# Optimization experiments

Measured on AMD Instinct MI355X. Metric: run time of the kernel, lower is better.

The kernel has to match this reference:

```python
import jax, jax.numpy as jnp
import numpy as np
import math

N_NODES = 50000
N_EDGES = 1600000
HIDDEN = 128
HEADS = 4
HEAD_DIM = HIDDEN // HEADS


def setup_inputs() -> dict:
    key = jax.random.key(0)
    ks = jax.random.split(key, 10)
    s_in = 1.0 / math.sqrt(4)
    s_out = 1.0 / math.sqrt(HIDDEN)
    return {
        "x": jax.random.normal(ks[0], (N_NODES, 4), dtype=jnp.float32),
        "edge_index": jax.random.randint(ks[1], (2, N_EDGES), 0, N_NODES, dtype=jnp.int32),
        "Wq": jax.random.uniform(ks[2], (HIDDEN, 4), jnp.float32, -s_in, s_in),
        "bq": jax.random.uniform(ks[3], (HIDDEN,), jnp.float32, -s_in, s_in),
        "Wk": jax.random.uniform(ks[4], (HIDDEN, 4), jnp.float32, -s_in, s_in),
        "bk": jax.random.uniform(ks[5], (HIDDEN,), jnp.float32, -s_in, s_in),
        "Wv": jax.random.uniform(ks[6], (HIDDEN, 4), jnp.float32, -s_in, s_in),
        "bv": jax.random.uniform(ks[7], (HIDDEN,), jnp.float32, -s_in, s_in),
        "Wo": jax.random.uniform(ks[8], (4, HIDDEN), jnp.float32, -s_out, s_out),
        "bo": jax.random.uniform(ks[9], (4,), jnp.float32, -s_out, s_out),
    }


def reference(x, edge_index, Wq, bq, Wk, bk, Wv, bv, Wo, bo):
    n = x.shape[0]
    # projections 4 -> hidden, split into heads: [N, H, D]
    Q = (x @ Wq.T + bq).reshape(n, HEADS, HEAD_DIM)
    K = (x @ Wk.T + bk).reshape(n, HEADS, HEAD_DIM)
    V = (x @ Wv.T + bv).reshape(n, HEADS, HEAD_DIM)
    row, col = edge_index[0], edge_index[1]
    # per-edge, per-head scores: [E, H]
    scores = jnp.einsum('ehd,ehd->eh', Q[row], K[col]) / math.sqrt(HEAD_DIM)
    # NB: original applies softmax over ALL edges (dim=0), per head
    w = jax.nn.softmax(scores, axis=0)  # [E, H]
    # attended[col] += w * V[row]  -> segment-sum over destination nodes
    contrib = w[:, :, None] * V[row]  # [E, H, D]
    attended = jax.ops.segment_sum(contrib, col, num_segments=n)  # [N, H, D]
    attended = attended.reshape(n, HIDDEN)
    out = attended @ Wo.T + bo  # dropout is identity in eval
    return out + x
```

## Files before the change

kernel.cpp:

```cpp
#include <hip/hip_runtime.h>
#include <math.h>

#define NNODES 50000
#define NEDGES 1600000
#define BINSZ 128
#define NBINS 391
#define NBLK 1000
#define EPB (NEDGES / NBLK)
#define HALF 500
#define PCAP 2560
#define SCALE 0.17677669529663687f

__device__ __forceinline__ void compute_C_entry(int t,
        const float* Wq, const float* bq, const float* Wk, const float* bk,
        const float* Wv, const float* bv, const float* Wo, float* C_lds) {
    if (t < 64) {
        int h = t >> 4, a = (t >> 2) & 3, b = t & 3;
        float s = 0.f;
        for (int k = 0; k < 32; k++) s += Wq[(h * 32 + k) * 4 + a] * Wk[(h * 32 + k) * 4 + b];
        C_lds[t] = s;
    } else if (t < 80) {
        int h = (t - 64) >> 2, b = (t - 64) & 3;
        float s = 0.f;
        for (int k = 0; k < 32; k++) s += bq[h * 32 + k] * Wk[(h * 32 + k) * 4 + b];
        C_lds[t] = s;
    } else if (t < 96) {
        int h = (t - 80) >> 2, a = (t - 80) & 3;
        float s = 0.f;
        for (int k = 0; k < 32; k++) s += Wq[(h * 32 + k) * 4 + a] * bk[h * 32 + k];
        C_lds[t] = s;
    } else if (t < 100) {
        int h = t - 96;
        float s = 0.f;
        for (int k = 0; k < 32; k++) s += bq[h * 32 + k] * bk[h * 32 + k];
        C_lds[t] = s;
    } else if (t < 164) {
        int i = t - 100;
        int h = i >> 4, o = (i >> 2) & 3, a = i & 3;
        float s = 0.f;
        for (int k = 0; k < 32; k++) s += Wo[o * 128 + h * 32 + k] * Wv[(h * 32 + k) * 4 + a];
        C_lds[t] = s;
    } else if (t < 180) {
        int i = t - 164;
        int h = i >> 2, o = i & 3;
        float s = 0.f;
        for (int k = 0; k < 32; k++) s += Wo[o * 128 + h * 32 + k] * bv[h * 32 + k];
        C_lds[t] = s;
    }
}

__global__ __launch_bounds__(256) void k_binA(const int* __restrict__ ei,
                                              unsigned* __restrict__ chunks,
                                              unsigned* __restrict__ dir) {
    __shared__ unsigned raw[EPB];
    __shared__ unsigned srt[EPB];
    __shared__ int hist[512];
    __shared__ int ofs[512];
    int t = threadIdx.x, blk = blockIdx.x;
    hist[t] = 0; hist[t + 256] = 0;
    __syncthreads();
    int e0 = blk * EPB;
    for (int i = t; i < EPB; i += 256) {
        int r = ei[e0 + i];
        int c = ei[NEDGES + e0 + i];
        raw[i] = ((unsigned)c << 16) | (unsigned)r;
        atomicAdd(&hist[c >> 7], 1);
    }
    __syncthreads();
    if (t < 64) {
        int v[8], run = 0;
#pragma unroll
        for (int j = 0; j < 8; j++) { v[j] = hist[8 * t + j]; run += v[j]; }
        int p = run;
#pragma unroll
        for (int off = 1; off < 64; off <<= 1) {
            int u = __shfl_up(p, off, 64);
            if (t >= off) p += u;
        }
        int base = p - run;
#pragma unroll
        for (int j = 0; j < 8; j++) {
            hist[8 * t + j] = base;
            ofs[8 * t + j] = base;
            base += v[j];
        }
    }
    __syncthreads();
    for (int i = t; i < EPB; i += 256) {
        unsigned v = raw[i];
        int pos = atomicAdd(&ofs[v >> 23], 1);
        srt[pos] = v;
    }
    __syncthreads();
    uint4* co = (uint4*)(chunks + (size_t)blk * EPB);
    const uint4* si = (const uint4*)srt;
    for (int i = t; i < EPB / 4; i += 256) co[i] = si[i];
    for (int b = t; b < NBINS; b += 256) {
        int start = hist[b];
        int len = ofs[b] - start;
        dir[(size_t)blk * NBINS + b] = ((unsigned)start << 16) | (unsigned)len;
    }
}

__global__ __launch_bounds__(256) void k_tr(const unsigned* __restrict__ dir,
                                            unsigned* __restrict__ dirT) {
    __shared__ unsigned tile[32][33];
    int bi = blockIdx.x % 13;
    int bj = blockIdx.x / 13;
    int tx = threadIdx.x & 31, ty = threadIdx.x >> 5;
    int col = bi * 32 + tx;
#pragma unroll
    for (int k = 0; k < 4; k++) {
        int row = bj * 32 + ty + k * 8;
        if (row < NBLK && col < NBINS) tile[ty + k * 8][tx] = dir[(size_t)row * NBINS + col];
    }
    __syncthreads();
    int col2 = bj * 32 + tx;
#pragma unroll
    for (int k = 0; k < 4; k++) {
        int row2 = bi * 32 + ty + k * 8;
        if (row2 < NBINS && col2 < NBLK) dirT[(size_t)row2 * NBLK + col2] = tile[tx][ty + k * 8];
    }
}

__global__ __launch_bounds__(256) void k_accum(
        const unsigned* __restrict__ chunks, const unsigned* __restrict__ dirT,
        const float* __restrict__ x,
        const float* __restrict__ Wq, const float* __restrict__ bq,
        const float* __restrict__ Wk, const float* __restrict__ bk,
        const float* __restrict__ Wv, const float* __restrict__ bv,
        const float* __restrict__ Wo,
        float* __restrict__ acc, float* __restrict__ pS) {
    __shared__ float Cl[192];
    __shared__ float pe[BINSZ][20];
    __shared__ unsigned raw[PCAP];
    __shared__ unsigned short srt[PCAP];
    __shared__ int hist[BINSZ];
    __shared__ int ofs[BINSZ];
    __shared__ int runStart[HALF];
    __shared__ int srcBase[HALF];
    __shared__ int wsum[4];
    __shared__ float sw[4][4];
    int bid = blockIdx.x;
    int bin = bid >> 1;
    int part = bid & 1;
    int t = threadIdx.x;
    int base = bin << 7;
    compute_C_entry(t, Wq, bq, Wk, bk, Wv, bv, Wo, Cl);
    if (t < BINSZ) hist[t] = 0;
    __syncthreads();
    if (t < BINSZ) {
        int node = base + t;
        if (node < NNODES) {
            float4 xv = ((const float4*)x)[node];
            float pr[20];
#pragma unroll
            for (int h = 0; h < 4; h++) {
#pragma unroll
                for (int a = 0; a < 4; a++) {
                    float g = Cl[80 + h * 4 + a]
                            + Cl[h * 16 + a * 4 + 0] * xv.x + Cl[h * 16 + a * 4 + 1] * xv.y
                            + Cl[h * 16 + a * 4 + 2] * xv.z + Cl[h * 16 + a * 4 + 3] * xv.w;
                    pr[h * 4 + a] = g * SCALE;
                }
                float e = Cl[96 + h]
                        + Cl[64 + h * 4 + 0] * xv.x + Cl[64 + h * 4 + 1] * xv.y
                        + Cl[64 + h * 4 + 2] * xv.z + Cl[64 + h * 4 + 3] * xv.w;
                pr[16 + h] = e * SCALE;
            }
#pragma unroll
            for (int q = 0; q < 5; q++) ((float4*)pe[t])[q] = ((const float4*)pr)[q];
        }
    }
    uint2 dd = {0u, 0u};
    int cnt = 0;
    if (t < HALF / 2) {
        dd = *(const uint2*)(dirT + (size_t)bin * NBLK + part * HALF + 2 * t);
        cnt = (int)(dd.x & 0xFFFFu) + (int)(dd.y & 0xFFFFu);
    }
    int lane = t & 63, w = t >> 6;
    int p = cnt;
#pragma unroll
    for (int off = 1; off < 64; off <<= 1) {
        int u = __shfl_up(p, off, 64);
        if (lane >= off) p += u;
    }
    if (lane == 63) wsum[w] = p;
    __syncthreads();
    int wbase = 0;
#pragma unroll
    for (int ww = 0; ww < 4; ww++) wbase += (ww < w) ? wsum[ww] : 0;
    int off0 = wbase + p - cnt;
    int nval = wsum[0] + wsum[1] + wsum[2] + wsum[3];
    if (nval > PCAP) nval = PCAP;
    if (t < HALF / 2) {
        int len0 = (int)(dd.x & 0xFFFFu);
        runStart[2 * t] = off0;
        runStart[2 * t + 1] = off0 + len0;
        srcBase[2 * t] = (part * HALF + 2 * t) * EPB + (int)(dd.x >> 16);
        srcBase[2 * t + 1] = (part * HALF + 2 * t + 1) * EPB + (int)(dd.y >> 16);
    }
    __syncthreads();
    for (int i = t; i < nval; i += 256) {
        int lo = 0, hi = HALF;
        while (hi - lo > 1) {
            int mid = (lo + hi) >> 1;
            if (runStart[mid] <= i) lo = mid; else hi = mid;
        }
        unsigned v = chunks[srcBase[lo] + (i - runStart[lo])];
        raw[i] = v;
        atomicAdd(&hist[(int)(v >> 16) - base], 1);
    }
    __syncthreads();
    if (t < 64) {
        int a0 = hist[2 * t], a1 = hist[2 * t + 1];
        int pair = a0 + a1;
        int pp = pair;
#pragma unroll
        for (int off = 1; off < 64; off <<= 1) {
            int u = __shfl_up(pp, off, 64);
            if (t >= off) pp += u;
        }
        int excl = pp - pair;
        hist[2 * t] = excl; hist[2 * t + 1] = excl + a0;
        ofs[2 * t] = excl;  ofs[2 * t + 1] = excl + a0;
    }
    __syncthreads();
    for (int i = t; i < nval; i += 256) {
        unsigned v = raw[i];
        int lc = (int)(v >> 16) - base;
        int pos = atomicAdd(&ofs[lc], 1);
        srt[pos] = (unsigned short)(v & 0xFFFFu);
    }
    __syncthreads();
    int nl = t >> 1;
    int sub = t & 1;
    int node = base + nl;
    int sBeg = hist[nl], sEnd = ofs[nl];
    float4 g0 = ((const float4*)pe[nl])[0];
    float4 g1 = ((const float4*)pe[nl])[1];
    float4 g2 = ((const float4*)pe[nl])[2];
    float4 g3 = ((const float4*)pe[nl])[3];
    float4 eh = ((const float4*)pe[nl])[4];
    float S0 = 0.f, S1 = 0.f, S2 = 0.f, S3 = 0.f;
    float4 y0 = {0, 0, 0, 0}, y1 = y0, y2 = y0, y3 = y0;
    for (int i = sBeg + sub; i < sEnd; i += 2) {
        int r = (int)srt[i];
        float4 xv = ((const float4*)x)[r];
        float p0 = __expf(xv.x * g0.x + xv.y * g0.y + xv.z * g0.z + xv.w * g0.w + eh.x);
        float p1 = __expf(xv.x * g1.x + xv.y * g1.y + xv.z * g1.z + xv.w * g1.w + eh.y);
        float p2 = __expf(xv.x * g2.x + xv.y * g2.y + xv.z * g2.z + xv.w * g2.w + eh.z);
        float p3 = __expf(xv.x * g3.x + xv.y * g3.y + xv.z * g3.z + xv.w * g3.w + eh.w);
        y0.x += p0 * xv.x; y0.y += p0 * xv.y; y0.z += p0 * xv.z; y0.w += p0 * xv.w;
        y1.x += p1 * xv.x; y1.y += p1 * xv.y; y1.z += p1 * xv.z; y1.w += p1 * xv.w;
        y2.x += p2 * xv.x; y2.y += p2 * xv.y; y2.z += p2 * xv.z; y2.w += p2 * xv.w;
        y3.x += p3 * xv.x; y3.y += p3 * xv.y; y3.z += p3 * xv.z; y3.w += p3 * xv.w;
        S0 += p0; S1 += p1; S2 += p2; S3 += p3;
    }
    y0.x += __shfl_xor(y0.x, 1); y0.y += __shfl_xor(y0.y, 1);
    y0.z += __shfl_xor(y0.z, 1); y0.w += __shfl_xor(y0.w, 1);
    y1.x += __shfl_xor(y1.x, 1); y1.y += __shfl_xor(y1.y, 1);
    y1.z += __shfl_xor(y1.z, 1); y1.w += __shfl_xor(y1.w, 1);
    y2.x += __shfl_xor(y2.x, 1); y2.y += __shfl_xor(y2.y, 1);
    y2.z += __shfl_xor(y2.z, 1); y2.w += __shfl_xor(y2.w, 1);
    y3.x += __shfl_xor(y3.x, 1); y3.y += __shfl_xor(y3.y, 1);
    y3.z += __shfl_xor(y3.z, 1); y3.w += __shfl_xor(y3.w, 1);
    S0 += __shfl_xor(S0, 1); S1 += __shfl_xor(S1, 1);
    S2 += __shfl_xor(S2, 1); S3 += __shfl_xor(S3, 1);
    if (node < NNODES) {
        float4* ap = (float4*)(acc + ((size_t)part * NNODES + node) * 20);
        float4 sv = {S0, S1, S2, S3};
        if (sub == 0) { ap[0] = y0; ap[2] = y2; ap[4] = sv; }
        else { ap[1] = y1; ap[3] = y3; }
    }
    float z0 = (sub == 0 && node < NNODES) ? S0 : 0.f;
    float z1 = (sub == 0 && node < NNODES) ? S1 : 0.f;
    float z2 = (sub == 0 && node < NNODES) ? S2 : 0.f;
    float z3 = (sub == 0 && node < NNODES) ? S3 : 0.f;
#pragma unroll
    for (int off = 1; off < 64; off <<= 1) {
        z0 += __shfl_xor(z0, off); z1 += __shfl_xor(z1, off);
        z2 += __shfl_xor(z2, off); z3 += __shfl_xor(z3, off);
    }
    if ((t & 63) == 0) { sw[w][0] = z0; sw[w][1] = z1; sw[w][2] = z2; sw[w][3] = z3; }
    __syncthreads();
    if (t == 0) {
        float4 v;
        v.x = sw[0][0] + sw[1][0] + sw[2][0] + sw[3][0];
        v.y = sw[0][1] + sw[1][1] + sw[2][1] + sw[3][1];
        v.z = sw[0][2] + sw[1][2] + sw[2][2] + sw[3][2];
        v.w = sw[0][3] + sw[1][3] + sw[2][3] + sw[3][3];
        ((float4*)pS)[bid] = v;
    }
}

__global__ __launch_bounds__(256) void k_out(
        const float* __restrict__ acc, const float* __restrict__ pS,
        const float* __restrict__ Wq, const float* __restrict__ bq,
        const float* __restrict__ Wk, const float* __restrict__ bk,
        const float* __restrict__ Wv, const float* __restrict__ bv,
        const float* __restrict__ Wo, const float* __restrict__ bo,
        const float* __restrict__ x, float* __restrict__ out) {
    __shared__ float Cl[192];
    __shared__ float sd[4][4];
    __shared__ float dd[4];
    int t = threadIdx.x;
    compute_C_entry(t, Wq, bq, Wk, bk, Wv, bv, Wo, Cl);
    float s0 = 0.f, s1 = 0.f, s2 = 0.f, s3 = 0.f;
    for (int i = t; i < 2 * NBINS; i += 256) {
        float4 v = ((const float4*)pS)[i];
        s0 += v.x; s1 += v.y; s2 += v.z; s3 += v.w;
    }
#pragma unroll
    for (int off = 1; off < 64; off <<= 1) {
        s0 += __shfl_xor(s0, off); s1 += __shfl_xor(s1, off);
        s2 += __shfl_xor(s2, off); s3 += __shfl_xor(s3, off);
    }
    int w = t >> 6;
    if ((t & 63) == 0) { sd[w][0] = s0; sd[w][1] = s1; sd[w][2] = s2; sd[w][3] = s3; }
    __syncthreads();
    if (t < 4) dd[t] = 1.f / (sd[0][t] + sd[1][t] + sd[2][t] + sd[3][t]);
    __syncthreads();
    int i = blockIdx.x * blockDim.x + t;
    if (i >= NNODES) return;
    const float4* a0 = (const float4*)(acc + (size_t)i * 20);
    const float4* a1 = (const float4*)(acc + ((size_t)NNODES + i) * 20);
    float4 y[4], S;
#pragma unroll
    for (int q = 0; q < 4; q++) {
        float4 u = a0[q], v = a1[q];
        y[q].x = u.x + v.x; y[q].y = u.y + v.y; y[q].z = u.z + v.z; y[q].w = u.w + v.w;
    }
    {
        float4 u = a0[4], v = a1[4];
        S.x = u.x + v.x; S.y = u.y + v.y; S.z = u.z + v.z; S.w = u.w + v.w;
    }
    float Sv[4] = {S.x, S.y, S.z, S.w};
    float di[4] = {dd[0], dd[1], dd[2], dd[3]};
    float o[4];
#pragma unroll
    for (int oo = 0; oo < 4; oo++) {
        float a = bo[oo];
#pragma unroll
        for (int h = 0; h < 4; h++) {
            float m = Cl[100 + h * 16 + oo * 4 + 0] * y[h].x
                    + Cl[100 + h * 16 + oo * 4 + 1] * y[h].y
                    + Cl[100 + h * 16 + oo * 4 + 2] * y[h].z
                    + Cl[100 + h * 16 + oo * 4 + 3] * y[h].w
                    + Cl[164 + h * 4 + oo] * Sv[h];
            a += di[h] * m;
        }
        o[oo] = a;
    }
    float4 xv = ((const float4*)x)[i];
    float4 ov;
    ov.x = o[0] + xv.x; ov.y = o[1] + xv.y; ov.z = o[2] + xv.z; ov.w = o[3] + xv.w;
    ((float4*)out)[i] = ov;
}

extern "C" void kernel_launch(void* const* d_in, const int* in_sizes, int n_in,
                              void* d_out, int out_size, void* d_ws, size_t ws_size,
                              hipStream_t stream) {
    const float* x = (const float*)d_in[0];
    const int* ei = (const int*)d_in[1];
    const float* Wq = (const float*)d_in[2];
    const float* bq = (const float*)d_in[3];
    const float* Wk = (const float*)d_in[4];
    const float* bk = (const float*)d_in[5];
    const float* Wv = (const float*)d_in[6];
    const float* bv = (const float*)d_in[7];
    const float* Wo = (const float*)d_in[8];
    const float* bo = (const float*)d_in[9];
    float* out = (float*)d_out;

    float* fws = (float*)d_ws;
    float* acc = fws;
    float* pS = acc + (size_t)2 * NNODES * 20;
    unsigned* chunks = (unsigned*)(pS + (size_t)2 * NBINS * 4 + 4);
    unsigned* dir = chunks + (size_t)NEDGES;
    unsigned* dirT = dir + (size_t)NBLK * NBINS;

    k_binA<<<NBLK, 256, 0, stream>>>(ei, chunks, dir);
    k_tr<<<13 * 32, 256, 0, stream>>>(dir, dirT);
    k_accum<<<2 * NBINS, 256, 0, stream>>>(chunks, dirT, x, Wq, bq, Wk, bk, Wv, bv, Wo, acc, pS);
    k_out<<<(NNODES + 255) / 256, 256, 0, stream>>>(acc, pS,
                                                    Wq, bq, Wk, bk, Wv, bv, Wo, bo, x, out);
}
```

Baseline: 52.78 us.

## Split accumulation into CSR-build kernel and node-split accumulate kernel

Before, each bin was split across two blocks by source-block half, and both partial results went to separate accumulator copies. Now a new kernel gathers every edge of a bin into a per-bin CSR, and the accumulate kernel splits a bin by node halves with four threads per node. The Q/K projections move into the transpose kernel, writing a global proj buffer. This drops the duplicate accumulator reads in k_out and the per-element binary search, at the cost of an extra launch and a CSR round-trip through global memory.

```diff
diff --git a/kernel.cpp b/kernel.cpp
--- a/kernel.cpp
+++ b/kernel.cpp
@@ -7,8 +7,8 @@
 #define NBINS 391
 #define NBLK 1000
 #define EPB (NEDGES / NBLK)
-#define HALF 500
-#define PCAP 2560
+#define CAPB 4864
+#define STRIP 19
 #define SCALE 0.17677669529663687f
 
 __device__ __forceinline__ void compute_C_entry(int t,
@@ -102,12 +102,18 @@
     }
 }
 
-__global__ __launch_bounds__(256) void k_tr(const unsigned* __restrict__ dir,
-                                            unsigned* __restrict__ dirT) {
+__global__ __launch_bounds__(256) void k_prep(const unsigned* __restrict__ dir,
+        unsigned* __restrict__ dirT, const float* __restrict__ x,
+        const float* __restrict__ Wq, const float* __restrict__ bq,
+        const float* __restrict__ Wk, const float* __restrict__ bk,
+        const float* __restrict__ Wv, const float* __restrict__ bv,
+        const float* __restrict__ Wo, float* __restrict__ proj) {
     __shared__ unsigned tile[32][33];
+    __shared__ float Cl[192];
+    int t = threadIdx.x;
     int bi = blockIdx.x % 13;
     int bj = blockIdx.x / 13;
-    int tx = threadIdx.x & 31, ty = threadIdx.x >> 5;
+    int tx = t & 31, ty = t >> 5;
     int col = bi * 32 + tx;
 #pragma unroll
     for (int k = 0; k < 4; k++) {
@@ -121,62 +127,50 @@
         int row2 = bi * 32 + ty + k * 8;
         if (row2 < NBINS && col2 < NBLK) dirT[(size_t)row2 * NBLK + col2] = tile[tx][ty + k * 8];
     }
-}
-
-__global__ __launch_bounds__(256) void k_accum(
-        const unsigned* __restrict__ chunks, const unsigned* __restrict__ dirT,
-        const float* __restrict__ x,
-        const float* __restrict__ Wq, const float* __restrict__ bq,
-        const float* __restrict__ Wk, const float* __restrict__ bk,
-        const float* __restrict__ Wv, const float* __restrict__ bv,
-        const float* __restrict__ Wo,
-        float* __restrict__ acc, float* __restrict__ pS) {
-    __shared__ float Cl[192];
-    __shared__ float pe[BINSZ][20];
-    __shared__ unsigned raw[PCAP];
-    __shared__ unsigned short srt[PCAP];
+    compute_C_entry(t, Wq, bq, Wk, bk, Wv, bv, Wo, Cl);
+    __syncthreads();
+    int i = blockIdx.x * 256 + t;
+    if (i >= NNODES) return;
+    float4 xv = ((const float4*)x)[i];
+    float pr[20];
+#pragma unroll
+    for (int h = 0; h < 4; h++) {
+#pragma unroll
+        for (int a = 0; a < 4; a++) {
+            float g = Cl[80 + h * 4 + a]
+                    + Cl[h * 16 + a * 4 + 0] * xv.x + Cl[h * 16 + a * 4 + 1] * xv.y
+                    + Cl[h * 16 + a * 4 + 2] * xv.z + Cl[h * 16 + a * 4 + 3] * xv.w;
+            pr[h * 4 + a] = g * SCALE;
+        }
+        float e = Cl[96 + h]
+                + Cl[64 + h * 4 + 0] * xv.x + Cl[64 + h * 4 + 1] * xv.y
+                + Cl[64 + h * 4 + 2] * xv.z + Cl[64 + h * 4 + 3] * xv.w;
+        pr[16 + h] = e * SCALE;
+    }
+    float4* pp = (float4*)(proj + (size_t)i * 20);
+#pragma unroll
+    for (int q = 0; q < 5; q++) pp[q] = ((const float4*)pr)[q];
+}
+
+__global__ __launch_bounds__(256) void k_csr(const unsigned* __restrict__ chunks,
+                                             const unsigned* __restrict__ dirT,
+                                             unsigned short* __restrict__ csr,
+                                             unsigned* __restrict__ rowptr) {
+    __shared__ unsigned raw[CAPB];
+    __shared__ unsigned short srt[CAPB];
+    __shared__ int runStart[NBLK + 1];
+    __shared__ int srcBase[NBLK];
     __shared__ int hist[BINSZ];
     __shared__ int ofs[BINSZ];
-    __shared__ int runStart[HALF];
-    __shared__ int srcBase[HALF];
     __shared__ int wsum[4];
-    __shared__ float sw[4][4];
-    int bid = blockIdx.x;
-    int bin = bid >> 1;
-    int part = bid & 1;
-    int t = threadIdx.x;
-    int base = bin << 7;
-    compute_C_entry(t, Wq, bq, Wk, bk, Wv, bv, Wo, Cl);
+    int bin = blockIdx.x, t = threadIdx.x;
     if (t < BINSZ) hist[t] = 0;
-    __syncthreads();
-    if (t < BINSZ) {
-        int node = base + t;
-        if (node < NNODES) {
-            float4 xv = ((const float4*)x)[node];
-            float pr[20];
-#pragma unroll
-            for (int h = 0; h < 4; h++) {
-#pragma unroll
-                for (int a = 0; a < 4; a++) {
-                    float g = Cl[80 + h * 4 + a]
-                            + Cl[h * 16 + a * 4 + 0] * xv.x + Cl[h * 16 + a * 4 + 1] * xv.y
-                            + Cl[h * 16 + a * 4 + 2] * xv.z + Cl[h * 16 + a * 4 + 3] * xv.w;
-                    pr[h * 4 + a] = g * SCALE;
-                }
-                float e = Cl[96 + h]
-                        + Cl[64 + h * 4 + 0] * xv.x + Cl[64 + h * 4 + 1] * xv.y
-                        + Cl[64 + h * 4 + 2] * xv.z + Cl[64 + h * 4 + 3] * xv.w;
-                pr[16 + h] = e * SCALE;
-            }
-#pragma unroll
-            for (int q = 0; q < 5; q++) ((float4*)pe[t])[q] = ((const float4*)pr)[q];
-        }
-    }
-    uint2 dd = {0u, 0u};
+    uint4 d4 = {0, 0, 0, 0};
     int cnt = 0;
-    if (t < HALF / 2) {
-        dd = *(const uint2*)(dirT + (size_t)bin * NBLK + part * HALF + 2 * t);
-        cnt = (int)(dd.x & 0xFFFFu) + (int)(dd.y & 0xFFFFu);
+    if (t < NBLK / 4) {
+        d4 = ((const uint4*)(dirT + (size_t)bin * NBLK))[t];
+        cnt = (int)(d4.x & 0xFFFFu) + (int)(d4.y & 0xFFFFu)
+            + (int)(d4.z & 0xFFFFu) + (int)(d4.w & 0xFFFFu);
     }
     int lane = t & 63, w = t >> 6;
     int p = cnt;
@@ -190,26 +184,37 @@
     int wbase = 0;
 #pragma unroll
     for (int ww = 0; ww < 4; ww++) wbase += (ww < w) ? wsum[ww] : 0;
-    int off0 = wbase + p - cnt;
+    int st = wbase + p - cnt;
     int nval = wsum[0] + wsum[1] + wsum[2] + wsum[3];
-    if (nval > PCAP) nval = PCAP;
-    if (t < HALF / 2) {
-        int len0 = (int)(dd.x & 0xFFFFu);
-        runStart[2 * t] = off0;
-        runStart[2 * t + 1] = off0 + len0;
-        srcBase[2 * t] = (part * HALF + 2 * t) * EPB + (int)(dd.x >> 16);
-        srcBase[2 * t + 1] = (part * HALF + 2 * t + 1) * EPB + (int)(dd.y >> 16);
-    }
-    __syncthreads();
-    for (int i = t; i < nval; i += 256) {
-        int lo = 0, hi = HALF;
+    if (nval > CAPB) nval = CAPB;
+    if (t < NBLK / 4) {
+        int l0 = d4.x & 0xFFFFu, l1 = d4.y & 0xFFFFu, l2 = d4.z & 0xFFFFu;
+        runStart[4 * t] = st;
+        runStart[4 * t + 1] = st + l0;
+        runStart[4 * t + 2] = st + l0 + l1;
+        runStart[4 * t + 3] = st + l0 + l1 + l2;
+        srcBase[4 * t]     = (4 * t) * EPB + (int)(d4.x >> 16);
+        srcBase[4 * t + 1] = (4 * t + 1) * EPB + (int)(d4.y >> 16);
+        srcBase[4 * t + 2] = (4 * t + 2) * EPB + (int)(d4.z >> 16);
+        srcBase[4 * t + 3] = (4 * t + 3) * EPB + (int)(d4.w >> 16);
+    }
+    if (t == 0) runStart[NBLK] = nval;
+    __syncthreads();
+    int i0 = t * STRIP;
+    int lim = i0 + STRIP; if (lim > nval) lim = nval;
+    if (i0 < lim) {
+        int lo = 0, hi = NBLK;
         while (hi - lo > 1) {
             int mid = (lo + hi) >> 1;
-            if (runStart[mid] <= i) lo = mid; else hi = mid;
-        }
-        unsigned v = chunks[srcBase[lo] + (i - runStart[lo])];
-        raw[i] = v;
-        atomicAdd(&hist[(int)(v >> 16) - base], 1);
+            if (runStart[mid] <= i0) lo = mid; else hi = mid;
+        }
+        int re = runStart[lo + 1];
+        for (int i = i0; i < lim; i++) {
+            while (i >= re) { lo++; re = runStart[lo + 1]; }
+            unsigned v = chunks[srcBase[lo] + (i - runStart[lo])];
+            raw[i] = v;
+            atomicAdd(&hist[(v >> 16) & 127], 1);
+        }
     }
     __syncthreads();
     if (t < 64) {
@@ -228,15 +233,43 @@
     __syncthreads();
     for (int i = t; i < nval; i += 256) {
         unsigned v = raw[i];
-        int lc = (int)(v >> 16) - base;
+        int lc = (v >> 16) & 127;
         int pos = atomicAdd(&ofs[lc], 1);
         srt[pos] = (unsigned short)(v & 0xFFFFu);
     }
     __syncthreads();
-    int nl = t >> 1;
-    int sub = t & 1;
+    unsigned* cd = (unsigned*)(csr + (size_t)bin * CAPB);
+    const unsigned* cs = (const unsigned*)srt;
+    int n32 = (nval + 1) >> 1;
+    for (int i = t; i < n32; i += 256) cd[i] = cs[i];
+    if (t < BINSZ) rowptr[bin * BINSZ + t] = ((unsigned)hist[t] << 16)
+                                           | (unsigned)(ofs[t] - hist[t]);
+}
+
+__global__ __launch_bounds__(256) void k_accum(const unsigned short* __restrict__ csr,
+        const unsigned* __restrict__ rowptr, const float* __restrict__ x,
+        const float* __restrict__ proj, float* __restrict__ acc,
+        float* __restrict__ pS) {
+    __shared__ float pe[64][20];
+    __shared__ float sw[4][4];
+    int bid = blockIdx.x;
+    int bin = bid >> 1;
+    int base = bin * BINSZ + (bid & 1) * 64;
+    int t = threadIdx.x;
+    {
+        const float4* ps = (const float4*)(proj + (size_t)base * 20);
+        int navail = NNODES - base;
+        int lim4 = (navail >= 64 ? 64 : navail) * 5;
+        float4* pd = (float4*)pe;
+        for (int i = t; i < lim4; i += 256) pd[i] = ps[i];
+    }
+    int nl = t >> 2;
+    int sub = t & 3;
     int node = base + nl;
-    int sBeg = hist[nl], sEnd = ofs[nl];
+    unsigned rp = (node < NNODES) ? rowptr[bin * BINSZ + (bid & 1) * 64 + nl] : 0u;
+    int st = rp >> 16, len = rp & 0xFFFFu;
+    __syncthreads();
+    const unsigned short* seg = csr + (size_t)bin * CAPB + st;
     float4 g0 = ((const float4*)pe[nl])[0];
     float4 g1 = ((const float4*)pe[nl])[1];
     float4 g2 = ((const float4*)pe[nl])[2];
@@ -244,8 +277,8 @@
     float4 eh = ((const float4*)pe[nl])[4];
     float S0 = 0.f, S1 = 0.f, S2 = 0.f, S3 = 0.f;
     float4 y0 = {0, 0, 0, 0}, y1 = y0, y2 = y0, y3 = y0;
-    for (int i = sBeg + sub; i < sEnd; i += 2) {
-        int r = (int)srt[i];
+    for (int i = sub; i < len; i += 4) {
+        int r = seg[i];
         float4 xv = ((const float4*)x)[r];
         float p0 = __expf(xv.x * g0.x + xv.y * g0.y + xv.z * g0.z + xv.w * g0.w + eh.x);
         float p1 = __expf(xv.x * g1.x + xv.y * g1.y + xv.z * g1.z + xv.w * g1.w + eh.y);
@@ -257,32 +290,37 @@
         y3.x += p3 * xv.x; y3.y += p3 * xv.y; y3.z += p3 * xv.z; y3.w += p3 * xv.w;
         S0 += p0; S1 += p1; S2 += p2; S3 += p3;
     }
-    y0.x += __shfl_xor(y0.x, 1); y0.y += __shfl_xor(y0.y, 1);
-    y0.z += __shfl_xor(y0.z, 1); y0.w += __shfl_xor(y0.w, 1);
-    y1.x += __shfl_xor(y1.x, 1); y1.y += __shfl_xor(y1.y, 1);
-    y1.z += __shfl_xor(y1.z, 1); y1.w += __shfl_xor(y1.w, 1);
-    y2.x += __shfl_xor(y2.x, 1); y2.y += __shfl_xor(y2.y, 1);
-    y2.z += __shfl_xor(y2.z, 1); y2.w += __shfl_xor(y2.w, 1);
-    y3.x += __shfl_xor(y3.x, 1); y3.y += __shfl_xor(y3.y, 1);
-    y3.z += __shfl_xor(y3.z, 1); y3.w += __shfl_xor(y3.w, 1);
-    S0 += __shfl_xor(S0, 1); S1 += __shfl_xor(S1, 1);
-    S2 += __shfl_xor(S2, 1); S3 += __shfl_xor(S3, 1);
+#pragma unroll
+    for (int off = 1; off < 4; off <<= 1) {
+        y0.x += __shfl_xor(y0.x, off); y0.y += __shfl_xor(y0.y, off);
+        y0.z += __shfl_xor(y0.z, off); y0.w += __shfl_xor(y0.w, off);
+        y1.x += __shfl_xor(y1.x, off); y1.y += __shfl_xor(y1.y, off);
+        y1.z += __shfl_xor(y1.z, off); y1.w += __shfl_xor(y1.w, off);
+        y2.x += __shfl_xor(y2.x, off); y2.y += __shfl_xor(y2.y, off);
+        y2.z += __shfl_xor(y2.z, off); y2.w += __shfl_xor(y2.w, off);
+        y3.x += __shfl_xor(y3.x, off); y3.y += __shfl_xor(y3.y, off);
+        y3.z += __shfl_xor(y3.z, off); y3.w += __shfl_xor(y3.w, off);
+        S0 += __shfl_xor(S0, off); S1 += __shfl_xor(S1, off);
+        S2 += __shfl_xor(S2, off); S3 += __shfl_xor(S3, off);
+    }
     if (node < NNODES) {
-        float4* ap = (float4*)(acc + ((size_t)part * NNODES + node) * 20);
-        float4 sv = {S0, S1, S2, S3};
-        if (sub == 0) { ap[0] = y0; ap[2] = y2; ap[4] = sv; }
-        else { ap[1] = y1; ap[3] = y3; }
+        float4* ap = (float4*)(acc + (size_t)node * 20);
+        if (sub == 0) { float4 sv = {S0, S1, S2, S3}; ap[0] = y0; ap[4] = sv; }
+        else if (sub == 1) ap[1] = y1;
+        else if (sub == 2) ap[2] = y2;
+        else ap[3] = y3;
     }
     float z0 = (sub == 0 && node < NNODES) ? S0 : 0.f;
     float z1 = (sub == 0 && node < NNODES) ? S1 : 0.f;
     float z2 = (sub == 0 && node < NNODES) ? S2 : 0.f;
     float z3 = (sub == 0 && node < NNODES) ? S3 : 0.f;
 #pragma unroll
-    for (int off = 1; off < 64; off <<= 1) {
+    for (int off = 4; off < 64; off <<= 1) {
         z0 += __shfl_xor(z0, off); z1 += __shfl_xor(z1, off);
         z2 += __shfl_xor(z2, off); z3 += __shfl_xor(z3, off);
     }
-    if ((t & 63) == 0) { sw[w][0] = z0; sw[w][1] = z1; sw[w][2] = z2; sw[w][3] = z3; }
+    int lane = t & 63, w = t >> 6;
+    if (lane == 0) { sw[w][0] = z0; sw[w][1] = z1; sw[w][2] = z2; sw[w][3] = z3; }
     __syncthreads();
     if (t == 0) {
         float4 v;
@@ -323,18 +361,9 @@
     __syncthreads();
     int i = blockIdx.x * blockDim.x + t;
     if (i >= NNODES) return;
-    const float4* a0 = (const float4*)(acc + (size_t)i * 20);
-    const float4* a1 = (const float4*)(acc + ((size_t)NNODES + i) * 20);
-    float4 y[4], S;
-#pragma unroll
-    for (int q = 0; q < 4; q++) {
-        float4 u = a0[q], v = a1[q];
-        y[q].x = u.x + v.x; y[q].y = u.y + v.y; y[q].z = u.z + v.z; y[q].w = u.w + v.w;
-    }
-    {
-        float4 u = a0[4], v = a1[4];
-        S.x = u.x + v.x; S.y = u.y + v.y; S.z = u.z + v.z; S.w = u.w + v.w;
-    }
+    const float4* ap = (const float4*)(acc + (size_t)i * 20);
+    float4 y[4] = {ap[0], ap[1], ap[2], ap[3]};
+    float4 S = ap[4];
     float Sv[4] = {S.x, S.y, S.z, S.w};
     float di[4] = {dd[0], dd[1], dd[2], dd[3]};
     float o[4];
@@ -375,14 +404,18 @@
 
     float* fws = (float*)d_ws;
     float* acc = fws;
-    float* pS = acc + (size_t)2 * NNODES * 20;
-    unsigned* chunks = (unsigned*)(pS + (size_t)2 * NBINS * 4 + 4);
+    float* pS = acc + (size_t)NNODES * 20;
+    float* proj = pS + 3200;
+    unsigned* chunks = (unsigned*)(proj + (size_t)NNODES * 20);
     unsigned* dir = chunks + (size_t)NEDGES;
     unsigned* dirT = dir + (size_t)NBLK * NBINS;
+    unsigned* rowptr = dirT + (size_t)NBINS * NBLK;
+    unsigned short* csr = (unsigned short*)(rowptr + (size_t)NBINS * BINSZ);
 
     k_binA<<<NBLK, 256, 0, stream>>>(ei, chunks, dir);
-    k_tr<<<13 * 32, 256, 0, stream>>>(dir, dirT);
-    k_accum<<<2 * NBINS, 256, 0, stream>>>(chunks, dirT, x, Wq, bq, Wk, bk, Wv, bv, Wo, acc, pS);
+    k_prep<<<13 * 32, 256, 0, stream>>>(dir, dirT, x, Wq, bq, Wk, bk, Wv, bv, Wo, proj);
+    k_csr<<<NBINS, 256, 0, stream>>>(chunks, dirT, csr, rowptr);
+    k_accum<<<2 * NBINS, 256, 0, stream>>>(csr, rowptr, x, proj, acc, pS);
     k_out<<<(NNODES + 255) / 256, 256, 0, stream>>>(acc, pS,
                                                     Wq, bq, Wk, bk, Wv, bv, Wo, bo, x, out);
 }
```

Result: slower. 57.69 us (+9.3%).
